# Kernel tuning notes

Hardware: AMD Instinct MI355X
Metric: run time of the kernel (lower is better)

Reference implementation:

```python
import jax, jax.numpy as jnp
import numpy as np

RO = 4.0
STRIDE = 1.0
DILATIONS = (1, 1, 1, 2, 2, 4, 4)  # deep-snake res blocks


def conv2d(x, w, b, pad):
    y = jax.lax.conv_general_dilated(x, w, (1, 1), [(pad, pad), (pad, pad)],
                                     dimension_numbers=('NCHW', 'OIHW', 'NCHW'))
    return y + b[None, :, None, None]


def circ_conv(x, w, b, dilation):
    # x: [N, C, V]; circular (wrap) padding of n_adj*dilation on each side, kernel size 9 (n_adj=4)
    pad = (w.shape[-1] // 2) * dilation
    xp = jnp.concatenate([x[..., -pad:], x, x[..., :pad]], axis=-1)
    y = jax.lax.conv_general_dilated(xp, w, (1,), 'VALID', rhs_dilation=(dilation,),
                                     dimension_numbers=('NCH', 'OIH', 'NCH'))
    return y + b[None, :, None]


def bn(x, gamma, beta):
    # BatchNorm1d in eval mode (running_mean=0, running_var=1)
    return x * gamma[None, :, None] + beta[None, :, None]


def conv1x1(x, w, b):
    return jnp.einsum('oc,ncv->nov', w, x) + b[None, :, None]


def grid_sample_polys(feat, polys, ind):
    # feat: [B, C, H, W]; polys: [N, V, 2] (x, y) in feature-map pixel coords; ind: [N]
    # torch grid_sample(bilinear, align_corners=False, zeros pad) after the deep-snake
    # normalization x/(w/2)-1 reduces to sampling at (px-0.5, py-0.5).
    B, C, H, W = feat.shape
    ix = polys[..., 0] - 0.5
    iy = polys[..., 1] - 0.5
    x0 = jnp.floor(ix)
    y0 = jnp.floor(iy)
    wx = (ix - x0)[..., None]
    wy = (iy - y0)[..., None]
    x0i = x0.astype(jnp.int32)
    y0i = y0.astype(jnp.int32)

    def gather(yi, xi):
        valid = (xi >= 0) & (xi < W) & (yi >= 0) & (yi < H)
        xc = jnp.clip(xi, 0, W - 1)
        yc = jnp.clip(yi, 0, H - 1)
        v = feat[ind[:, None], :, yc, xc]  # [N, V, C]
        return v * valid[..., None]

    v00 = gather(y0i, x0i)
    v01 = gather(y0i, x0i + 1)
    v10 = gather(y0i + 1, x0i)
    v11 = gather(y0i + 1, x0i + 1)
    out = (v00 * (1 - wx) * (1 - wy) + v01 * wx * (1 - wy)
           + v10 * (1 - wx) * wy + v11 * wx * wy)
    return out.transpose(0, 2, 1)  # [N, C, V]


def snake_forward(x, head_w, head_b, head_g, head_bt, res_w, res_b, res_g, res_bt,
                  fus_w, fus_b, pw1, pb1, pw2, pb2, pw3, pb3):
    # Deep-snake Snake with conv_type='dgrid': head + 7 residual dilated circular convs,
    # fusion 1x1 + global max pool, then 3-layer 1x1 prediction head -> 2 offsets.
    h = bn(jax.nn.relu(circ_conv(x, head_w, head_b, 1)), head_g, head_bt)
    states = [h]
    cur = h
    for i, d in enumerate(DILATIONS):
        y = bn(jax.nn.relu(circ_conv(cur, res_w[i], res_b[i], d)), res_g[i], res_bt[i])
        cur = y + cur
        states.append(cur)
    state = jnp.concatenate(states, axis=1)  # [N, 8*state_dim, V]
    g = conv1x1(state, fus_w, fus_b)
    g = jnp.max(g, axis=2, keepdims=True)
    g = jnp.broadcast_to(g, (state.shape[0], g.shape[1], state.shape[2]))
    s = jnp.concatenate([g, state], axis=1)
    h1 = jax.nn.relu(conv1x1(s, pw1, pb1))
    h2 = jax.nn.relu(conv1x1(h1, pw2, pb2))
    return conv1x1(h2, pw3, pb3)  # [N, 2, V]


def setup_inputs() -> dict:
    key = jax.random.key(0)
    ks = jax.random.split(key, 24)
    B, C_IN, H, W = 8, 66, 128, 128
    NP, V = 128, 128
    SD = 128           # Snake state_dim = num_vertex
    FD = 66            # snake feature_dim = c_out_proj + 2
    K = 9              # 2*n_adj + 1
    nres = len(DILATIONS)
    s = 0.01  # torch init: normal_(0, 0.01)
    inp = {
        'cnn_feature': jax.random.normal(ks[0], (B, C_IN, H, W), jnp.float32),
        'i_it_poly': jax.random.uniform(ks[1], (NP, V, 2), jnp.float32) * (W - 1),
        'c_it_poly': jax.random.normal(ks[2], (NP, V, 2), jnp.float32) * 0.25,
        'ind': jax.random.randint(ks[3], (NP,), 0, B, jnp.int32),
        'proj_w1': jax.random.normal(ks[4], (256, C_IN, 3, 3), jnp.float32) * s,
        'proj_b1': jnp.zeros((256,), jnp.float32),
        'proj_w2': jax.random.normal(ks[5], (64, 256, 1, 1), jnp.float32) * s,
        'proj_b2': jnp.zeros((64,), jnp.float32),
        'head_w': jax.random.normal(ks[6], (SD, FD, K), jnp.float32) * s,
        'head_b': jnp.zeros((SD,), jnp.float32),
        'head_g': jnp.ones((SD,), jnp.float32),
        'head_bt': jnp.zeros((SD,), jnp.float32),
        'res_w': jax.random.normal(ks[7], (nres, SD, SD, K), jnp.float32) * s,
        'res_b': jnp.zeros((nres, SD), jnp.float32),
        'res_g': jnp.ones((nres, SD), jnp.float32),
        'res_bt': jnp.zeros((nres, SD), jnp.float32),
        'fus_w': jax.random.normal(ks[8], (256, SD * (nres + 1)), jnp.float32) * s,
        'fus_b': jnp.zeros((256,), jnp.float32),
        'pw1': jax.random.normal(ks[9], (256, SD * (nres + 1) + 256), jnp.float32) * s,
        'pb1': jnp.zeros((256,), jnp.float32),
        'pw2': jax.random.normal(ks[10], (64, 256), jnp.float32) * s,
        'pb2': jnp.zeros((64,), jnp.float32),
        'pw3': jax.random.normal(ks[11], (2, 64), jnp.float32) * s,
        'pb3': jnp.zeros((2,), jnp.float32),
    }
    return inp


def reference(cnn_feature, i_it_poly, c_it_poly, ind,
              proj_w1, proj_b1, proj_w2, proj_b2,
              head_w, head_b, head_g, head_bt,
              res_w, res_b, res_g, res_bt,
              fus_w, fus_b, pw1, pb1, pw2, pb2, pw3, pb3):
    # projection: conv3x3 -> relu -> conv1x1  (66 -> 256 -> 64)
    feat = jax.nn.relu(conv2d(cnn_feature, proj_w1, proj_b1, 1))
    feat = conv2d(feat, proj_w2, proj_b2, 0)
    # gather per-vertex features via bilinear grid sampling (get_gcn_feature)
    vert_feat = grid_sample_polys(feat, i_it_poly, ind)          # [N, 64, V]
    coords = (c_it_poly * RO).transpose(0, 2, 1)                  # [N, 2, V]
    init_input = jnp.concatenate([vert_feat, coords], axis=1)     # [N, 66, V]
    offset = snake_forward(init_input, head_w, head_b, head_g, head_bt,
                           res_w, res_b, res_g, res_bt,
                           fus_w, fus_b, pw1, pb1, pw2, pb2, pw3, pb3)
    i_poly = i_it_poly * RO + offset.transpose(0, 2, 1) * STRIDE  # [N, V, 2]
    return i_poly
```

## Files before the change

### kernel.cpp

```cpp
#include <hip/hip_runtime.h>
#include <hip/hip_bf16.h>

constexpr int B   = 8;
constexpr int CIN = 66;
constexpr int H   = 128, W = 128;
constexpr int C1  = 256;
constexpr int NP  = 128;
constexpr int V   = 128;
constexpr int SD  = 128;
constexpr int NRES = 7;
constexpr float RO = 4.0f;

typedef __bf16 bf16x8 __attribute__((ext_vector_type(8)));
typedef float  f32x4  __attribute__((ext_vector_type(4)));
typedef unsigned short u16x8 __attribute__((ext_vector_type(8)));

__device__ inline float bfu2f(unsigned short u) {
    union { unsigned int i; float f; } c; c.i = ((unsigned)u) << 16; return c.f;
}

__global__ __launch_bounds__(256) void k_pack_x(const float* __restrict__ x,
                                                __hip_bfloat16* __restrict__ xp)
{
    const int bi  = blockIdx.x;
    const int b   = bi / 130;
    const int yp  = bi % 130;
    const int tid = threadIdx.x;
    const int y   = yp - 1;
    const bool interior = (y >= 0 && y < H);

    __shared__ float xs[CIN * W];
    if (interior) {
        for (int i = tid; i < CIN * W; i += 256)
            xs[i] = x[((size_t)b * CIN + (i >> 7)) * (H * W) + y * W + (i & 127)];
    }
    __syncthreads();
    __hip_bfloat16* op = xp + ((size_t)b * 130 + yp) * (130 * 72);
    for (int i = tid; i < 130 * 72; i += 256) {
        int xpx = i / 72, c = i - xpx * 72;
        int xx = xpx - 1;
        float v = 0.f;
        if (interior && xx >= 0 && xx < W && c < CIN) v = xs[c * W + xx];
        op[i] = __float2bfloat16(v);
    }
}

__global__ __launch_bounds__(256) void k_pack_weights(
    const float* __restrict__ w3, const float* __restrict__ hw,
    const float* __restrict__ rw, const float* __restrict__ fw,
    const float* __restrict__ ppw1, const float* __restrict__ ppw2,
    __hip_bfloat16* __restrict__ wp2, __hip_bfloat16* __restrict__ wpk2,
    __hip_bfloat16* __restrict__ fwb, __hip_bfloat16* __restrict__ pw1hb,
    __hip_bfloat16* __restrict__ pw2b)
{
    const int bid = blockIdx.x, tid = threadIdx.x;
    if (bid < 256) {
        int oc = bid, ocg = bid >> 6, ocl = bid & 63;
        for (int t = tid; t < 3 * 232; t += 256) {
            int ky = t / 232, s = t - ky * 232;
            float v = 0.f;
            if (s < 216) {
                int kx = s / 72, ic = s - kx * 72;
                if (ic < CIN) v = w3[((size_t)(oc * CIN + ic) * 3 + ky) * 3 + kx];
            }
            wp2[(((size_t)ky * 4 + ocg) * 64 + ocl) * 232 + s] = __float2bfloat16(v);
        }
    } else if (bid < 1280) {
        int q = bid - 256, l = q >> 7, oc = q & 127;
        for (int t = tid; t < 9 * 128; t += 256) {
            int k = t >> 7, ic = t & 127;
            float v = 0.f;
            if (l == 0) { if (ic < 66) v = hw[((size_t)oc * 66 + ic) * 9 + k]; }
            else v = rw[((((size_t)(l - 1) * 128 + oc) * 128) + ic) * 9 + k];
            wpk2[(((size_t)l * 9 + k) * 128 + oc) * 128 + ic] = __float2bfloat16(v);
        }
    } else if (bid < 1536) {
        int r = bid - 1280;
        for (int c = tid; c < 1024; c += 256)
            fwb[(size_t)r * 1024 + c] = __float2bfloat16(fw[(size_t)r * 1024 + c]);
    } else if (bid < 1792) {
        int r = bid - 1536;
        for (int c = tid; c < 1024; c += 256)
            pw1hb[(size_t)r * 1024 + c] = __float2bfloat16(ppw1[(size_t)r * 1280 + 256 + c]);
    } else {
        int r = bid - 1792;
        for (int c = tid; c < 256; c += 256)
            pw2b[(size_t)r * 256 + c] = __float2bfloat16(ppw2[(size_t)r * 256 + c]);
    }
}

__global__ __launch_bounds__(256) void k_conv3x3_mfma(
    const __hip_bfloat16* __restrict__ xp,
    const __hip_bfloat16* __restrict__ wp2,
    const float* __restrict__ bias,
    __hip_bfloat16* __restrict__ out)
{
    __shared__ __hip_bfloat16 ash[28112];
    __shared__ __hip_bfloat16 bsh[2 * 14848];

    const int tid = threadIdx.x;
    const int ln  = tid & 63;
    const int wv  = tid >> 6;
    const int wm  = (wv >> 1) * 64;
    const int wn  = (wv & 1) * 32;
    const int l15 = ln & 15;
    const int lhi = ln >> 4;

    const int by  = blockIdx.x;
    const int b   = by >> 7;
    const int y   = by & 127;
    const int ocg = blockIdx.y;
    const int ocb = ocg * 64;

    {
        const char* g = (const char*)(xp + ((size_t)b * 130 + y) * 9360);
        for (int off = tid * 16; off < 56160; off += 4096)
            __builtin_amdgcn_global_load_lds(
                (const __attribute__((address_space(1))) void*)(g + off),
                (__attribute__((address_space(3))) void*)((char*)ash + off), 16, 0, 0);
        const char* gb = (const char*)(wp2 + ((size_t)0 * 4 + ocg) * 14848);
        for (int off = tid * 16; off < 29696; off += 4096)
            __builtin_amdgcn_global_load_lds(
                (const __attribute__((address_space(1))) void*)(gb + off),
                (__attribute__((address_space(3))) void*)((char*)bsh + off), 16, 0, 0);
        if (tid < 32) ash[28080 + tid] = __float2bfloat16(0.f);
    }
    __syncthreads();

    f32x4 acc[4][2] = {};
#pragma unroll
    for (int ky = 0; ky < 3; ++ky) {
        if (ky < 2) {
            const char* gb = (const char*)(wp2 + ((size_t)(ky + 1) * 4 + ocg) * 14848);
            char* dst = (char*)bsh + ((ky + 1) & 1) * 29696;
            for (int off = tid * 16; off < 29696; off += 4096)
                __builtin_amdgcn_global_load_lds(
                    (const __attribute__((address_space(1))) void*)(gb + off),
                    (__attribute__((address_space(3))) void*)(dst + off), 16, 0, 0);
        }
        const char* arow = (const char*)ash + ky * 18720;
        const char* bb   = (const char*)bsh + (ky & 1) * 29696;
#pragma unroll
        for (int ks = 0; ks < 7; ++ks) {
            bf16x8 a[4], bq[2];
#pragma unroll
            for (int m = 0; m < 4; ++m)
                a[m] = *(const bf16x8*)(arow + (wm + m * 16 + l15) * 144 + ks * 64 + lhi * 16);
#pragma unroll
            for (int n = 0; n < 2; ++n)
                bq[n] = *(const bf16x8*)(bb + (wn + n * 16 + l15) * 464 + ks * 64 + lhi * 16);
#pragma unroll
            for (int m = 0; m < 4; ++m)
#pragma unroll
                for (int n = 0; n < 2; ++n)
                    acc[m][n] = __builtin_amdgcn_mfma_f32_16x16x32_bf16(
                        a[m], bq[n], acc[m][n], 0, 0, 0);
        }
        __syncthreads();
    }

#pragma unroll
    for (int n = 0; n < 2; ++n) {
        int oc = ocb + wn + n * 16 + l15;
        float bb = bias[oc];
#pragma unroll
        for (int m = 0; m < 4; ++m) {
#pragma unroll
            for (int r = 0; r < 4; ++r) {
                int pos = wm + m * 16 + lhi * 4 + r;
                float v = acc[m][n][r] + bb;
                v = v > 0.f ? v : 0.f;
                out[(((size_t)b * 128 + y) * 128 + pos) * 256 + oc] = __float2bfloat16(v);
            }
        }
    }
}

__global__ __launch_bounds__(256) void k_conv1x1_mfma(
    const __hip_bfloat16* __restrict__ feat1,
    const __hip_bfloat16* __restrict__ w2b,
    const float* __restrict__ b2,
    __hip_bfloat16* __restrict__ feat2)
{
    const int tid = threadIdx.x;
    const int ln  = tid & 63;
    const int wv  = tid >> 6;
    const int wm  = wv * 64;
    const int l15 = ln & 15;
    const int lhi = ln >> 4;
    const int pos0 = blockIdx.x * 256;

    __shared__ __hip_bfloat16 wsh[64 * 136];
    for (int i = tid; i < 1024; i += 256) {
        int row = i >> 4, slot = i & 15;
        *(bf16x8*)&wsh[row * 136 + slot * 8] = *(const bf16x8*)(w2b + row * 256 + slot * 8);
    }
    __syncthreads();

    f32x4 acc[4][4] = {};
#pragma unroll
    for (int kk = 0; kk < 8; ++kk) {
        bf16x8 a[4], bq[4];
#pragma unroll
        for (int m = 0; m < 4; ++m)
            a[m] = *(const bf16x8*)(feat1 + (size_t)(pos0 + wm + m * 16 + l15) * 256 + kk * 32 + lhi * 8);
#pragma unroll
        for (int n = 0; n < 4; ++n)
            bq[n] = *(const bf16x8*)&wsh[(n * 16 + l15) * 136 + kk * 32 + lhi * 8];
#pragma unroll
        for (int m = 0; m < 4; ++m)
#pragma unroll
            for (int n = 0; n < 4; ++n)
                acc[m][n] = __builtin_amdgcn_mfma_f32_16x16x32_bf16(a[m], bq[n], acc[m][n], 0, 0, 0);
    }
#pragma unroll
    for (int n = 0; n < 4; ++n) {
        int og = n * 16 + l15;
        float bb = b2[og];
#pragma unroll
        for (int m = 0; m < 4; ++m)
#pragma unroll
            for (int r = 0; r < 4; ++r) {
                int pos = pos0 + wm + m * 16 + lhi * 4 + r;
                feat2[(size_t)pos * 64 + og] = __float2bfloat16(acc[m][n][r] + bb);
            }
    }
}

__global__ __launch_bounds__(256) void k_sample(
    const __hip_bfloat16* __restrict__ feat2, const float* __restrict__ ipoly,
    const float* __restrict__ cpoly, const int* __restrict__ ind,
    __hip_bfloat16* __restrict__ X0)
{
    const int p = blockIdx.x;
    const int v = threadIdx.x & 127;
    const int half = threadIdx.x >> 7;

    float px = ipoly[(p * V + v) * 2 + 0];
    float py = ipoly[(p * V + v) * 2 + 1];
    float ix = px - 0.5f, iy = py - 0.5f;
    float x0f = floorf(ix), y0f = floorf(iy);
    float wx = ix - x0f, wy = iy - y0f;
    int x0 = (int)x0f, y0 = (int)y0f;

    int   xsv[2] = {x0, x0 + 1}, ysv[2] = {y0, y0 + 1};
    float wxs[2] = {1.f - wx, wx}, wys[2] = {1.f - wy, wy};
    float cw[4]; int cbase[4];
#pragma unroll
    for (int jy = 0; jy < 2; ++jy)
#pragma unroll
        for (int jx = 0; jx < 2; ++jx) {
            int xi = xsv[jx], yi = ysv[jy];
            bool ok = (xi >= 0) && (xi < W) && (yi >= 0) && (yi < H);
            int xc = min(max(xi, 0), W - 1);
            int yc = min(max(yi, 0), H - 1);
            cw[jy * 2 + jx]    = wys[jy] * wxs[jx] * (ok ? 1.f : 0.f);
            cbase[jy * 2 + jx] = yc * W + xc;
        }

    const __hip_bfloat16* fb = feat2 + (size_t)ind[p] * (16384 * 64);
    __hip_bfloat16* xr = X0 + ((size_t)p * V + v) * 128;
#pragma unroll
    for (int ch = 0; ch < 4; ++ch) {
        int chh = half * 4 + ch;
        float s[8];
#pragma unroll
        for (int e = 0; e < 8; ++e) s[e] = 0.f;
#pragma unroll
        for (int j = 0; j < 4; ++j) {
            u16x8 t = *(const u16x8*)(fb + (size_t)cbase[j] * 64 + chh * 8);
#pragma unroll
            for (int e = 0; e < 8; ++e) s[e] += cw[j] * bfu2f(t[e]);
        }
#pragma unroll
        for (int e = 0; e < 8; ++e) xr[chh * 8 + e] = __float2bfloat16(s[e]);
    }
    if (half) {
        xr[64] = __float2bfloat16(cpoly[(p * V + v) * 2 + 0] * RO);
        xr[65] = __float2bfloat16(cpoly[(p * V + v) * 2 + 1] * RO);
        for (int c = 66; c < 128; ++c) xr[c] = __float2bfloat16(0.f);
    }
}

__global__ __launch_bounds__(256) void k_snake_mfma(
    const __hip_bfloat16* __restrict__ xin,
    const __hip_bfloat16* __restrict__ wl,
    const float* __restrict__ bias, const float* __restrict__ gamma,
    const float* __restrict__ beta,
    const __hip_bfloat16* __restrict__ resin,
    __hip_bfloat16* __restrict__ out,
    int dil)
{
    const int tid = threadIdx.x;
    const int ln  = tid & 63;
    const int wv  = tid >> 6;
    const int wm  = (wv >> 1) * 32;
    const int wn  = (wv & 1) * 32;
    const int l15 = ln & 15;
    const int lhi = ln >> 4;
    const int p   = blockIdx.x;
    const int mg  = blockIdx.y >> 1;
    const int og  = blockIdx.y & 1;
    const int pos0 = mg * 64;
    const int ocb  = og * 64;

    __shared__ __hip_bfloat16 xs[96 * 136];
    const __hip_bfloat16* xb = xin + (size_t)p * (V * 128);
    for (int i = tid; i < 96 * 16; i += 256) {
        int r = i >> 4, slot = i & 15;
        int grow = (pos0 - 16 + r) & 127;
        *(bf16x8*)&xs[r * 136 + slot * 8] = *(const bf16x8*)(xb + (size_t)grow * 128 + slot * 8);
    }
    __syncthreads();

    f32x4 acc[2][2] = {};
#pragma unroll 1
    for (int k = 0; k < 9; ++k) {
        const int ofs = (k - 4) * dil + 16;
        const __hip_bfloat16* wk = wl + (size_t)k * (128 * 128);
#pragma unroll
        for (int kc = 0; kc < 4; ++kc) {
            bf16x8 a[2], bq[2];
#pragma unroll
            for (int m = 0; m < 2; ++m) {
                int row = wm + m * 16 + l15 + ofs;
                a[m] = *(const bf16x8*)&xs[row * 136 + kc * 32 + lhi * 8];
            }
#pragma unroll
            for (int n = 0; n < 2; ++n)
                bq[n] = *(const bf16x8*)(wk + (size_t)(ocb + wn + n * 16 + l15) * 128 + kc * 32 + lhi * 8);
#pragma unroll
            for (int m = 0; m < 2; ++m)
#pragma unroll
                for (int n = 0; n < 2; ++n)
                    acc[m][n] = __builtin_amdgcn_mfma_f32_16x16x32_bf16(a[m], bq[n], acc[m][n], 0, 0, 0);
        }
    }

#pragma unroll
    for (int n = 0; n < 2; ++n) {
        int oc = ocb + wn + n * 16 + l15;
        float bb = bias[oc], gg = gamma[oc], bt = beta[oc];
#pragma unroll
        for (int m = 0; m < 2; ++m)
#pragma unroll
            for (int r = 0; r < 4; ++r) {
                int pos = pos0 + wm + m * 16 + lhi * 4 + r;
                size_t idx = ((size_t)p * V + pos) * 128 + oc;
                float v = acc[m][n][r] + bb;
                v = v > 0.f ? v : 0.f;
                v = v * gg + bt;
                if (resin) v += __bfloat162float(resin[idx]);
                out[idx] = __float2bfloat16(v);
            }
    }
}

__global__ __launch_bounds__(256) void k_vconv1024(
    const __hip_bfloat16* __restrict__ xin,
    const __hip_bfloat16* __restrict__ wb,
    const float* __restrict__ fbias,
    const float* __restrict__ pbias,
    int relu,
    __hip_bfloat16* __restrict__ out)
{
    const int tid = threadIdx.x;
    const int ln  = tid & 63;
    const int wv  = tid >> 6;
    const int wm  = (wv >> 1) * 64;
    const int wn  = (wv & 1) * 64;
    const int l15 = ln & 15;
    const int lhi = ln >> 4;
    const int p   = blockIdx.x;
    const int ocb = blockIdx.y * 128;

    f32x4 acc[4][4] = {};
    for (int s = 0; s < 8; ++s) {
        const __hip_bfloat16* xa = xin + ((size_t)s * NP + p) * (V * 128);
#pragma unroll
        for (int kc = 0; kc < 4; ++kc) {
            bf16x8 a[4], bq[4];
#pragma unroll
            for (int m = 0; m < 4; ++m)
                a[m] = *(const bf16x8*)(xa + (size_t)(wm + m * 16 + l15) * 128 + kc * 32 + lhi * 8);
#pragma unroll
            for (int n = 0; n < 4; ++n)
                bq[n] = *(const bf16x8*)(wb + (size_t)(ocb + wn + n * 16 + l15) * 1024 + s * 128 + kc * 32 + lhi * 8);
#pragma unroll
            for (int m = 0; m < 4; ++m)
#pragma unroll
                for (int n = 0; n < 4; ++n)
                    acc[m][n] = __builtin_amdgcn_mfma_f32_16x16x32_bf16(a[m], bq[n], acc[m][n], 0, 0, 0);
        }
    }
#pragma unroll
    for (int n = 0; n < 4; ++n) {
        int og = ocb + wn + n * 16 + l15;
        float bb = (fbias ? fbias[og] : 0.f) + (pbias ? pbias[(size_t)p * 256 + og] : 0.f);
#pragma unroll
        for (int m = 0; m < 4; ++m)
#pragma unroll
            for (int r = 0; r < 4; ++r) {
                int pos = wm + m * 16 + lhi * 4 + r;
                float v = acc[m][n][r] + bb;
                if (relu) v = v > 0.f ? v : 0.f;
                out[((size_t)p * V + pos) * 256 + og] = __float2bfloat16(v);
            }
    }
}

__global__ __launch_bounds__(128) void k_h2(
    const __hip_bfloat16* __restrict__ h1,
    const __hip_bfloat16* __restrict__ w2b,
    const float* __restrict__ pb2,
    __hip_bfloat16* __restrict__ h2)
{
    const int tid = threadIdx.x;
    const int ln  = tid & 63;
    const int wv  = tid >> 6;
    const int wm  = wv * 64;
    const int l15 = ln & 15;
    const int lhi = ln >> 4;
    const int p   = blockIdx.x;

    f32x4 acc[4][4] = {};
#pragma unroll
    for (int kk = 0; kk < 8; ++kk) {
        bf16x8 a[4], bq[4];
#pragma unroll
        for (int m = 0; m < 4; ++m)
            a[m] = *(const bf16x8*)(h1 + ((size_t)p * V + wm + m * 16 + l15) * 256 + kk * 32 + lhi * 8);
#pragma unroll
        for (int n = 0; n < 4; ++n)
            bq[n] = *(const bf16x8*)(w2b + (size_t)(n * 16 + l15) * 256 + kk * 32 + lhi * 8);
#pragma unroll
        for (int m = 0; m < 4; ++m)
#pragma unroll
            for (int n = 0; n < 4; ++n)
                acc[m][n] = __builtin_amdgcn_mfma_f32_16x16x32_bf16(a[m], bq[n], acc[m][n], 0, 0, 0);
    }
#pragma unroll
    for (int n = 0; n < 4; ++n) {
        int og = n * 16 + l15;
        float bb = pb2[og];
#pragma unroll
        for (int m = 0; m < 4; ++m)
#pragma unroll
            for (int r = 0; r < 4; ++r) {
                int pos = wm + m * 16 + lhi * 4 + r;
                float v = acc[m][n][r] + bb;
                v = v > 0.f ? v : 0.f;
                h2[((size_t)p * V + pos) * 64 + og] = __float2bfloat16(v);
            }
    }
}

__global__ __launch_bounds__(256) void k_gmaxgc(const __hip_bfloat16* __restrict__ fused,
                                                const float* __restrict__ pw1,
                                                const float* __restrict__ pb1,
                                                float* __restrict__ gc)
{
    int p = blockIdx.x, o = threadIdx.x;
    float m = -3.4e38f;
    for (int v = 0; v < V; ++v)
        m = fmaxf(m, __bfloat162float(fused[((size_t)p * V + v) * 256 + o]));
    __shared__ float gl[256];
    gl[o] = m;
    __syncthreads();
    float a = pb1[o];
    const float* wr = pw1 + (size_t)o * 1280;
    for (int c = 0; c < 256; ++c) a += wr[c] * gl[c];
    gc[(size_t)p * 256 + o] = a;
}

__global__ __launch_bounds__(128) void k_final(const __hip_bfloat16* __restrict__ h2,
                                               const float* __restrict__ pw3,
                                               const float* __restrict__ pb3,
                                               const float* __restrict__ ipoly,
                                               float* __restrict__ outp)
{
    int p = blockIdx.x, v = threadIdx.x;
    __shared__ float w3[128];
    w3[v] = pw3[v];
    __syncthreads();
    float a0 = pb3[0], a1 = pb3[1];
    const u16x8* hp = (const u16x8*)(h2 + ((size_t)p * V + v) * 64);
#pragma unroll
    for (int ch = 0; ch < 8; ++ch) {
        u16x8 t = hp[ch];
#pragma unroll
        for (int e = 0; e < 8; ++e) {
            int c = ch * 8 + e;
            float hv = bfu2f(t[e]);
            a0 += w3[c] * hv;
            a1 += w3[64 + c] * hv;
        }
    }
    int idx = (p * V + v) * 2;
    outp[idx]     = ipoly[idx] * RO + a0;
    outp[idx + 1] = ipoly[idx + 1] * RO + a1;
}

extern "C" void kernel_launch(void* const* d_in, const int* in_sizes, int n_in,
                              void* d_out, int out_size, void* d_ws, size_t ws_size,
                              hipStream_t stream)
{
    const float* cnn   = (const float*)d_in[0];
    const float* ipoly = (const float*)d_in[1];
    const float* cpoly = (const float*)d_in[2];
    const int*   ind   = (const int*)d_in[3];
    const float* pw1c  = (const float*)d_in[4];
    const float* pb1c  = (const float*)d_in[5];
    const float* pw2c  = (const float*)d_in[6];
    const float* pb2c  = (const float*)d_in[7];
    const float* hw    = (const float*)d_in[8];
    const float* hb    = (const float*)d_in[9];
    const float* hg    = (const float*)d_in[10];
    const float* hbt   = (const float*)d_in[11];
    const float* rw    = (const float*)d_in[12];
    const float* rb    = (const float*)d_in[13];
    const float* rg    = (const float*)d_in[14];
    const float* rbt   = (const float*)d_in[15];
    const float* fw    = (const float*)d_in[16];
    const float* fb    = (const float*)d_in[17];
    const float* ppw1  = (const float*)d_in[18];
    const float* ppb1  = (const float*)d_in[19];
    const float* ppw2  = (const float*)d_in[20];
    const float* ppb2  = (const float*)d_in[21];
    const float* ppw3  = (const float*)d_in[22];
    const float* ppb3  = (const float*)d_in[23];
    float* outp = (float*)d_out;

    char* ws = (char*)d_ws;
    __hip_bfloat16* feat1  = (__hip_bfloat16*)(ws);
    __hip_bfloat16* states = (__hip_bfloat16*)(ws);
    __hip_bfloat16* fused  = (__hip_bfloat16*)(ws + 33554432);
    __hip_bfloat16* h1     = (__hip_bfloat16*)(ws + 41943040);
    __hip_bfloat16* h2     = (__hip_bfloat16*)(ws + 50331648);
    float*          gcbuf  = (float*)(ws + 52428800);
    __hip_bfloat16* xp     = (__hip_bfloat16*)(ws + 67108864);
    __hip_bfloat16* feat2  = (__hip_bfloat16*)(ws + 67108864);
    __hip_bfloat16* wp2    = (__hip_bfloat16*)(ws + 86577664);
    __hip_bfloat16* wpk2   = (__hip_bfloat16*)(ws + 86934016);
    __hip_bfloat16* fwb    = (__hip_bfloat16*)(ws + 89293312);
    __hip_bfloat16* pw1hb  = (__hip_bfloat16*)(ws + 89817600);
    __hip_bfloat16* pw2b   = (__hip_bfloat16*)(ws + 90341888);
    __hip_bfloat16* X0     = (__hip_bfloat16*)(ws + 90374656);

    k_pack_x<<<dim3(8 * 130), 256, 0, stream>>>(cnn, xp);
    k_pack_weights<<<dim3(1856), 256, 0, stream>>>(pw1c, hw, rw, fw, ppw1, ppw2,
                                                   wp2, wpk2, fwb, pw1hb, pw2b);

    k_conv3x3_mfma<<<dim3(1024, 4), 256, 0, stream>>>(xp, wp2, pb1c, feat1);
    k_conv1x1_mfma<<<dim3(512), 256, 0, stream>>>(feat1, pw2b, pb2c, feat2);
    k_sample<<<dim3(NP), 256, 0, stream>>>(feat2, ipoly, cpoly, ind, X0);

    k_snake_mfma<<<dim3(NP, 4), 256, 0, stream>>>(X0, wpk2, hb, hg, hbt, nullptr,
                                                  states, 1);
    const int dil[NRES] = {1, 1, 1, 2, 2, 4, 4};
    const size_t SSZ = (size_t)NP * V * 128;
    for (int i = 0; i < NRES; ++i) {
        const __hip_bfloat16* xin = states + (size_t)i * SSZ;
        __hip_bfloat16* yout      = states + (size_t)(i + 1) * SSZ;
        const __hip_bfloat16* wi  = wpk2 + (size_t)(i + 1) * 9 * 128 * 128;
        k_snake_mfma<<<dim3(NP, 4), 256, 0, stream>>>(xin, wi, rb + i * SD, rg + i * SD,
                                                      rbt + i * SD, xin, yout, dil[i]);
    }

    k_vconv1024<<<dim3(NP, 2), 256, 0, stream>>>(states, fwb, fb, nullptr, 0, fused);
    k_gmaxgc<<<dim3(NP), 256, 0, stream>>>(fused, ppw1, ppb1, gcbuf);
    k_vconv1024<<<dim3(NP, 2), 256, 0, stream>>>(states, pw1hb, nullptr, gcbuf, 1, h1);
    k_h2<<<dim3(NP), 128, 0, stream>>>(h1, pw2b, ppb2, h2);
    k_final<<<dim3(NP), 128, 0, stream>>>(h2, ppw3, ppb3, ipoly, outp);
}
```

Before: 556.7 us.

## Retile conv3x3 and snake convs with LDS-staged weights and swizzle

The 3x3 projection conv now uses 128-channel output tiles, so there are half as many blocks. It loads one input row and one weight slab per ky step into smaller LDS buffers, which drops the double buffering and hints two blocks per CU. The snake conv now keeps all 128 vertices per block and wraps rows with a modulo, so the circular halo no longer needs a separate load. Its weights are double-buffered in LDS with an XOR-swizzled layout, written by the pack kernel, to avoid bank conflicts in place of direct global loads. The costs are fewer blocks for both kernels, which hurts occupancy, and extra synchronisation per step.

```diff
diff --git a/kernel.cpp b/kernel.cpp
--- a/kernel.cpp
+++ b/kernel.cpp
@@ -55,7 +55,7 @@
 {
     const int bid = blockIdx.x, tid = threadIdx.x;
     if (bid < 256) {
-        int oc = bid, ocg = bid >> 6, ocl = bid & 63;
+        int oc = bid;
         for (int t = tid; t < 3 * 232; t += 256) {
             int ky = t / 232, s = t - ky * 232;
             float v = 0.f;
@@ -63,7 +63,7 @@
                 int kx = s / 72, ic = s - kx * 72;
                 if (ic < CIN) v = w3[((size_t)(oc * CIN + ic) * 3 + ky) * 3 + kx];
             }
-            wp2[(((size_t)ky * 4 + ocg) * 64 + ocl) * 232 + s] = __float2bfloat16(v);
+            wp2[((size_t)ky * 256 + oc) * 232 + s] = __float2bfloat16(v);
         }
     } else if (bid < 1280) {
         int q = bid - 256, l = q >> 7, oc = q & 127;
@@ -72,7 +72,9 @@
             float v = 0.f;
             if (l == 0) { if (ic < 66) v = hw[((size_t)oc * 66 + ic) * 9 + k]; }
             else v = rw[((((size_t)(l - 1) * 128 + oc) * 128) + ic) * 9 + k];
-            wpk2[(((size_t)l * 9 + k) * 128 + oc) * 128 + ic] = __float2bfloat16(v);
+            int s = ic >> 3, j = ic & 7;
+            int sw = ((s ^ (oc & 7)) << 3) + j;
+            wpk2[(((size_t)l * 9 + k) * 128 + oc) * 128 + sw] = __float2bfloat16(v);
         }
     } else if (bid < 1536) {
         int r = bid - 1280;
@@ -89,78 +91,83 @@
     }
 }
 
-__global__ __launch_bounds__(256) void k_conv3x3_mfma(
+__global__ __launch_bounds__(256, 2) void k_conv3x3_mfma(
     const __hip_bfloat16* __restrict__ xp,
-    const __hip_bfloat16* __restrict__ wp2,
+    const __hip_bfloat16* __restrict__ wp,
     const float* __restrict__ bias,
     __hip_bfloat16* __restrict__ out)
 {
-    __shared__ __hip_bfloat16 ash[28112];
-    __shared__ __hip_bfloat16 bsh[2 * 14848];
+    constexpr int SB = 232;
+    __shared__ __hip_bfloat16 ash[9392];
+    __shared__ __hip_bfloat16 bsh[128 * SB];
 
     const int tid = threadIdx.x;
     const int ln  = tid & 63;
     const int wv  = tid >> 6;
     const int wm  = (wv >> 1) * 64;
-    const int wn  = (wv & 1) * 32;
+    const int wn  = (wv & 1) * 64;
     const int l15 = ln & 15;
     const int lhi = ln >> 4;
 
     const int by  = blockIdx.x;
     const int b   = by >> 7;
     const int y   = by & 127;
-    const int ocg = blockIdx.y;
-    const int ocb = ocg * 64;
-
-    {
-        const char* g = (const char*)(xp + ((size_t)b * 130 + y) * 9360);
-        for (int off = tid * 16; off < 56160; off += 4096)
-            __builtin_amdgcn_global_load_lds(
-                (const __attribute__((address_space(1))) void*)(g + off),
-                (__attribute__((address_space(3))) void*)((char*)ash + off), 16, 0, 0);
-        const char* gb = (const char*)(wp2 + ((size_t)0 * 4 + ocg) * 14848);
-        for (int off = tid * 16; off < 29696; off += 4096)
-            __builtin_amdgcn_global_load_lds(
-                (const __attribute__((address_space(1))) void*)(gb + off),
-                (__attribute__((address_space(3))) void*)((char*)bsh + off), 16, 0, 0);
-        if (tid < 32) ash[28080 + tid] = __float2bfloat16(0.f);
-    }
-    __syncthreads();
-
-    f32x4 acc[4][2] = {};
-#pragma unroll
+    const int ocb = blockIdx.y * 128;
+
+    if (tid < 32) ash[9360 + tid] = __float2bfloat16(0.f);
+
+    f32x4 acc[4][4] = {};
+
     for (int ky = 0; ky < 3; ++ky) {
-        if (ky < 2) {
-            const char* gb = (const char*)(wp2 + ((size_t)(ky + 1) * 4 + ocg) * 14848);
-            char* dst = (char*)bsh + ((ky + 1) & 1) * 29696;
-            for (int off = tid * 16; off < 29696; off += 4096)
-                __builtin_amdgcn_global_load_lds(
-                    (const __attribute__((address_space(1))) void*)(gb + off),
-                    (__attribute__((address_space(3))) void*)(dst + off), 16, 0, 0);
-        }
-        const char* arow = (const char*)ash + ky * 18720;
-        const char* bb   = (const char*)bsh + (ky & 1) * 29696;
+        __syncthreads();
+        {
+            const char* g = (const char*)(xp + ((size_t)b * 130 + y + ky) * 9360);
+            for (int off = wv * 1024; off < 18720; off += 4096) {
+                int o = off + ln * 16;
+                if (o < 18720)
+                    __builtin_amdgcn_global_load_lds(
+                        (const __attribute__((address_space(1))) void*)(g + o),
+                        (__attribute__((address_space(3))) void*)((char*)ash + off),
+                        16, 0, 0);
+            }
+        }
+        {
+            const char* g = (const char*)(wp + ((size_t)ky * 256 + ocb) * SB);
+            for (int off = wv * 1024; off < 59392; off += 4096) {
+                int o = off + ln * 16;
+                if (o < 59392)
+                    __builtin_amdgcn_global_load_lds(
+                        (const __attribute__((address_space(1))) void*)(g + o),
+                        (__attribute__((address_space(3))) void*)((char*)bsh + off),
+                        16, 0, 0);
+            }
+        }
+        __syncthreads();
+
 #pragma unroll
         for (int ks = 0; ks < 7; ++ks) {
-            bf16x8 a[4], bq[2];
+            bf16x8 a[4], bq[4];
+#pragma unroll
+            for (int m = 0; m < 4; ++m) {
+                int pos = wm + m * 16 + l15;
+                a[m] = *(const bf16x8*)((const char*)ash + pos * 144 + ks * 64 + lhi * 16);
+            }
+#pragma unroll
+            for (int n = 0; n < 4; ++n) {
+                int oc = wn + n * 16 + l15;
+                bq[n] = *(const bf16x8*)((const char*)bsh + oc * (SB * 2) + ks * 64 + lhi * 16);
+            }
 #pragma unroll
             for (int m = 0; m < 4; ++m)
-                a[m] = *(const bf16x8*)(arow + (wm + m * 16 + l15) * 144 + ks * 64 + lhi * 16);
-#pragma unroll
-            for (int n = 0; n < 2; ++n)
-                bq[n] = *(const bf16x8*)(bb + (wn + n * 16 + l15) * 464 + ks * 64 + lhi * 16);
-#pragma unroll
-            for (int m = 0; m < 4; ++m)
-#pragma unroll
-                for (int n = 0; n < 2; ++n)
+#pragma unroll
+                for (int n = 0; n < 4; ++n)
                     acc[m][n] = __builtin_amdgcn_mfma_f32_16x16x32_bf16(
                         a[m], bq[n], acc[m][n], 0, 0, 0);
         }
-        __syncthreads();
-    }
-
-#pragma unroll
-    for (int n = 0; n < 2; ++n) {
+    }
+
+#pragma unroll
+    for (int n = 0; n < 4; ++n) {
         int oc = ocb + wn + n * 16 + l15;
         float bb = bias[oc];
 #pragma unroll
@@ -294,47 +301,64 @@
     const int tid = threadIdx.x;
     const int ln  = tid & 63;
     const int wv  = tid >> 6;
-    const int wm  = (wv >> 1) * 32;
+    const int wm  = (wv >> 1) * 64;
     const int wn  = (wv & 1) * 32;
     const int l15 = ln & 15;
     const int lhi = ln >> 4;
     const int p   = blockIdx.x;
-    const int mg  = blockIdx.y >> 1;
-    const int og  = blockIdx.y & 1;
-    const int pos0 = mg * 64;
-    const int ocb  = og * 64;
-
-    __shared__ __hip_bfloat16 xs[96 * 136];
+    const int ocb = blockIdx.y * 64;
+
+    __shared__ __hip_bfloat16 xs[128 * 136];
+    __shared__ __hip_bfloat16 wsh[2 * 64 * 128];
+
+    {
+        const char* g = (const char*)(wl + (size_t)ocb * 128);
+        for (int off = tid * 16; off < 16384; off += 4096)
+            __builtin_amdgcn_global_load_lds(
+                (const __attribute__((address_space(1))) void*)(g + off),
+                (__attribute__((address_space(3))) void*)((char*)wsh + off), 16, 0, 0);
+    }
     const __hip_bfloat16* xb = xin + (size_t)p * (V * 128);
-    for (int i = tid; i < 96 * 16; i += 256) {
+    for (int i = tid; i < 2048; i += 256) {
         int r = i >> 4, slot = i & 15;
-        int grow = (pos0 - 16 + r) & 127;
-        *(bf16x8*)&xs[r * 136 + slot * 8] = *(const bf16x8*)(xb + (size_t)grow * 128 + slot * 8);
+        *(bf16x8*)&xs[r * 136 + slot * 8] = *(const bf16x8*)(xb + r * 128 + slot * 8);
     }
     __syncthreads();
 
-    f32x4 acc[2][2] = {};
+    f32x4 acc[4][2] = {};
 #pragma unroll 1
     for (int k = 0; k < 9; ++k) {
-        const int ofs = (k - 4) * dil + 16;
-        const __hip_bfloat16* wk = wl + (size_t)k * (128 * 128);
+        if (k < 8) {
+            const char* g = (const char*)(wl + (size_t)(k + 1) * (128 * 128) + (size_t)ocb * 128);
+            char* dst = (char*)wsh + ((k + 1) & 1) * 16384;
+            for (int off = tid * 16; off < 16384; off += 4096)
+                __builtin_amdgcn_global_load_lds(
+                    (const __attribute__((address_space(1))) void*)(g + off),
+                    (__attribute__((address_space(3))) void*)(dst + off), 16, 0, 0);
+        }
+        const __hip_bfloat16* wbuf = wsh + (k & 1) * 8192;
+        const int ofs = (k - 4) * dil + 256;
 #pragma unroll
         for (int kc = 0; kc < 4; ++kc) {
-            bf16x8 a[2], bq[2];
-#pragma unroll
-            for (int m = 0; m < 2; ++m) {
-                int row = wm + m * 16 + l15 + ofs;
+            bf16x8 a[4], bq[2];
+#pragma unroll
+            for (int m = 0; m < 4; ++m) {
+                int row = (wm + m * 16 + l15 + ofs) & 127;
                 a[m] = *(const bf16x8*)&xs[row * 136 + kc * 32 + lhi * 8];
             }
 #pragma unroll
-            for (int n = 0; n < 2; ++n)
-                bq[n] = *(const bf16x8*)(wk + (size_t)(ocb + wn + n * 16 + l15) * 128 + kc * 32 + lhi * 8);
-#pragma unroll
-            for (int m = 0; m < 2; ++m)
+            for (int n = 0; n < 2; ++n) {
+                int row  = wn + n * 16 + l15;
+                int slot = (kc * 4 + lhi) ^ (row & 7);
+                bq[n] = *(const bf16x8*)&wbuf[row * 128 + slot * 8];
+            }
+#pragma unroll
+            for (int m = 0; m < 4; ++m)
 #pragma unroll
                 for (int n = 0; n < 2; ++n)
                     acc[m][n] = __builtin_amdgcn_mfma_f32_16x16x32_bf16(a[m], bq[n], acc[m][n], 0, 0, 0);
         }
+        __syncthreads();
     }
 
 #pragma unroll
@@ -342,10 +366,10 @@
         int oc = ocb + wn + n * 16 + l15;
         float bb = bias[oc], gg = gamma[oc], bt = beta[oc];
 #pragma unroll
-        for (int m = 0; m < 2; ++m)
+        for (int m = 0; m < 4; ++m)
 #pragma unroll
             for (int r = 0; r < 4; ++r) {
-                int pos = pos0 + wm + m * 16 + lhi * 4 + r;
+                int pos = wm + m * 16 + lhi * 4 + r;
                 size_t idx = ((size_t)p * V + pos) * 128 + oc;
                 float v = acc[m][n][r] + bb;
                 v = v > 0.f ? v : 0.f;
@@ -551,11 +575,11 @@
     k_pack_weights<<<dim3(1856), 256, 0, stream>>>(pw1c, hw, rw, fw, ppw1, ppw2,
                                                    wp2, wpk2, fwb, pw1hb, pw2b);
 
-    k_conv3x3_mfma<<<dim3(1024, 4), 256, 0, stream>>>(xp, wp2, pb1c, feat1);
+    k_conv3x3_mfma<<<dim3(1024, 2), 256, 0, stream>>>(xp, wp2, pb1c, feat1);
     k_conv1x1_mfma<<<dim3(512), 256, 0, stream>>>(feat1, pw2b, pb2c, feat2);
     k_sample<<<dim3(NP), 256, 0, stream>>>(feat2, ipoly, cpoly, ind, X0);
 
-    k_snake_mfma<<<dim3(NP, 4), 256, 0, stream>>>(X0, wpk2, hb, hg, hbt, nullptr,
+    k_snake_mfma<<<dim3(NP, 2), 256, 0, stream>>>(X0, wpk2, hb, hg, hbt, nullptr,
                                                   states, 1);
     const int dil[NRES] = {1, 1, 1, 2, 2, 4, 4};
     const size_t SSZ = (size_t)NP * V * 128;
@@ -563,7 +587,7 @@
         const __hip_bfloat16* xin = states + (size_t)i * SSZ;
         __hip_bfloat16* yout      = states + (size_t)(i + 1) * SSZ;
         const __hip_bfloat16* wi  = wpk2 + (size_t)(i + 1) * 9 * 128 * 128;
-        k_snake_mfma<<<dim3(NP, 4), 256, 0, stream>>>(xin, wi, rb + i * SD, rg + i * SD,
+        k_snake_mfma<<<dim3(NP, 2), 256, 0, stream>>>(xin, wi, rb + i * SD, rg + i * SD,
                                                       rbt + i * SD, xin, yout, dil[i]);
     }
 
```

After: 453.1 us. 1.23x faster.
